# Performance work log

Hardware: AMD Instinct MI355X
Metric: run time of the kernel (lower is better)

## Reference

```python
import jax, jax.numpy as jnp
import numpy as np

N = 2048       # num_nodes
B = 32         # batch
UNITS = 64     # rnn_units
OUT_DIM = 1
K = 2          # max_diffusion_step


def _rw(a):
    # random-walk matrix D^-1 A
    d = a.sum(axis=1, keepdims=True)
    return a / jnp.maximum(d, 1e-8)


def _supports(adj):
    # dual_random_walk: forward and backward random-walk transitions (transposed, as in DCRNN)
    return [_rw(adj).T, _rw(adj.T).T]


def _gconv(supports, x_bnf, w, b):
    # x_bnf: (B, N, F). Faithful to DCRNN: x0 columns are F-major then B,
    # and x0/x1 are rebound across supports exactly like the original loop.
    B_, N_, F_ = x_bnf.shape
    x0 = x_bnf.transpose(1, 2, 0).reshape(N_, F_ * B_)
    xs = [x0]
    for S in supports:
        x1 = S @ x0
        xs.append(x1)
        for _ in range(2, K + 1):
            x2 = 2.0 * (S @ x1) - x0
            xs.append(x2)
            x1, x0 = x2, x1
    M = len(xs)  # num_supports*K + 1 = 5
    x = jnp.stack(xs).reshape(M, N_, F_, B_).transpose(3, 1, 2, 0).reshape(B_ * N_, F_ * M)
    return x @ w + b


def _cell(supports, inp_flat, hx_flat, wg, bg, wc, bc):
    B_ = inp_flat.shape[0]
    inp = inp_flat.reshape(B_, N, -1)
    hx = hx_flat.reshape(B_, N, UNITS)
    cat = jnp.concatenate([inp, hx], axis=-1)
    val = jax.nn.sigmoid(_gconv(supports, cat, wg, bg)).reshape(B_, N, 2 * UNITS)
    r, u = val[..., :UNITS], val[..., UNITS:]
    c = jnp.tanh(_gconv(supports, jnp.concatenate([inp, r * hx], axis=-1), wc, bc).reshape(B_, N, UNITS))
    h = u * hx + (1.0 - u) * c
    return h.reshape(B_, N * UNITS)


def setup_inputs() -> dict:
    key = jax.random.key(0)
    ks = jax.random.split(key, 10)
    s = 0.02
    return {
        "inputs": jax.random.normal(ks[0], (B, N * OUT_DIM), jnp.float32),
        "hidden_state": jax.random.normal(ks[1], (2, B, N * UNITS), jnp.float32),
        "adj_mx": jax.random.uniform(ks[2], (N, N), jnp.float32),
        "w_gate_0": jax.random.normal(ks[3], ((1 + UNITS) * 5, 2 * UNITS), jnp.float32) * s,
        "b_gate_0": jnp.ones((2 * UNITS,), jnp.float32),
        "w_cand_0": jax.random.normal(ks[4], ((1 + UNITS) * 5, UNITS), jnp.float32) * s,
        "b_cand_0": jnp.zeros((UNITS,), jnp.float32),
        "w_gate_1": jax.random.normal(ks[5], ((UNITS + UNITS) * 5, 2 * UNITS), jnp.float32) * s,
        "b_gate_1": jnp.ones((2 * UNITS,), jnp.float32),
        "w_cand_1": jax.random.normal(ks[6], ((UNITS + UNITS) * 5, UNITS), jnp.float32) * s,
        "b_cand_1": jnp.zeros((UNITS,), jnp.float32),
        "w_proj": jax.random.normal(ks[7], (UNITS, OUT_DIM), jnp.float32) * s,
        "b_proj": jnp.zeros((OUT_DIM,), jnp.float32),
    }


def reference(inputs, hidden_state, adj_mx, w_gate_0, b_gate_0, w_cand_0, b_cand_0,
              w_gate_1, b_gate_1, w_cand_1, b_cand_1, w_proj, b_proj):
    supports = _supports(adj_mx)
    h0 = _cell(supports, inputs, hidden_state[0], w_gate_0, b_gate_0, w_cand_0, b_cand_0)
    h1 = _cell(supports, h0, hidden_state[1], w_gate_1, b_gate_1, w_cand_1, b_cand_1)
    out = (h1.reshape(-1, UNITS) @ w_proj + b_proj).reshape(-1, N * OUT_DIM)
    return out, jnp.stack([h0, h1])
```

## Files before the change

### kernel.cpp

```cpp
#include <hip/hip_runtime.h>

typedef unsigned short u16;
typedef unsigned char u8;
typedef unsigned int u32;
typedef float f32x4 __attribute__((ext_vector_type(4)));
typedef __bf16 bf16x8 __attribute__((ext_vector_type(8)));
typedef int i32x8 __attribute__((ext_vector_type(8)));

#define SCL_A 0x77777777
#define SCL_B 0x7F7F7F7F

__device__ __forceinline__ u16 f2bf(float f){
  u32 u = __builtin_bit_cast(u32, f);
  u32 r = (u + 0x7fffu + ((u >> 16) & 1u)) >> 16;
  return (u16)r;
}
__device__ __forceinline__ float bf2f(u16 h){
  return __builtin_bit_cast(float, ((u32)h) << 16);
}
__device__ __forceinline__ u8 f2e4(float x){
  return (u8)(__builtin_amdgcn_cvt_pk_fp8_f32(x, x, 0, false) & 0xff);
}
__device__ __forceinline__ u32 pack4_e4(float a, float b, float c, float d){
  int w = __builtin_amdgcn_cvt_pk_fp8_f32(a, b, 0, false);
  w = __builtin_amdgcn_cvt_pk_fp8_f32(c, d, w, true);
  return (u32)w;
}
__device__ __forceinline__ void gl_lds16(const void* g, void* l){
  __builtin_amdgcn_global_load_lds((__attribute__((address_space(1))) void*)g,
                                   (__attribute__((address_space(3))) void*)l,
                                   16, 0, 0);
}
__device__ __forceinline__ float sigf(float x){ return 1.f/(1.f + __expf(-x)); }

__device__ __forceinline__ void xcd_swizzle(int& x, int& y, int& z){
  int gx = gridDim.x, gy = gridDim.y;
  int nwg = gx * gy * gridDim.z;
  int lid = blockIdx.x + gx*(blockIdx.y + gy*blockIdx.z);
  int cpx = nwg >> 3;
  int swz = (lid & 7)*cpx + (lid >> 3);
  x = swz % gx;
  int rest = swz / gx;
  y = rest % gy;
  z = rest / gy;
}

__global__ __launch_bounds__(256) void k_rowsum(const float* __restrict__ adj, float* __restrict__ inv_rs,
                                                float* __restrict__ cs){
  int j = blockIdx.x; int tid = threadIdx.x;
  float s = 0.f;
  for (int i = tid; i < 2048; i += 256) s += adj[(long)j*2048 + i];
  for (int off = 32; off; off >>= 1) s += __shfl_down(s, off, 64);
  __shared__ float red[4];
  if ((tid & 63) == 0) red[tid >> 6] = s;
  __syncthreads();
  if (tid == 0){
    float t = red[0] + red[1] + red[2] + red[3];
    inv_rs[j] = 1.f / fmaxf(t, 1e-8f);
    cs[j] = 0.f;
  }
}

__global__ __launch_bounds__(256) void k_colsum2(const float* __restrict__ adj, float* __restrict__ cs){
  int j0 = blockIdx.x * 64, i0 = blockIdx.y * 128;
  int jj = threadIdx.x & 63, w = threadIdx.x >> 6;
  float s = 0.f;
  for (int i = w; i < 128; i += 4) s += adj[(long)(i0+i)*2048 + j0 + jj];
  __shared__ float red[256];
  red[threadIdx.x] = s;
  __syncthreads();
  if (w == 0){
    float t = red[jj] + red[64+jj] + red[128+jj] + red[192+jj];
    atomicAdd(&cs[j0+jj], t);
  }
}

__global__ __launch_bounds__(256) void k_build_S(const float* __restrict__ adj,
                                                 const float* __restrict__ inv_rs,
                                                 const float* __restrict__ cs,
                                                 u16* __restrict__ S0, u8* __restrict__ S0q,
                                                 u16* __restrict__ S0T, u16* __restrict__ S1){
  __shared__ float t[64*66];
  __shared__ float rsl[64];
  __shared__ float icl[64];
  int i0 = blockIdx.x * 64, j0 = blockIdx.y * 64;
  int tid = threadIdx.x;
  if (tid < 64) rsl[tid] = inv_rs[j0 + tid];
  else if (tid >= 64 && tid < 128) icl[tid-64] = 1.f / fmaxf(cs[i0 + tid-64], 1e-8f);
  __syncthreads();
  for (int e = tid; e < 4096; e += 256){
    int jj = e >> 6, ii = e & 63;
    float a = adj[(long)(j0+jj)*2048 + i0 + ii];
    t[jj*66 + ii] = a;
    long o = (long)(j0+jj)*2048 + i0 + ii;
    S0T[o] = f2bf(a * rsl[jj]);
    S1[o]  = f2bf(a * icl[ii]);
  }
  __syncthreads();
  for (int e = tid; e < 4096; e += 256){
    int ii = e >> 6, jj = e & 63;
    u16 vb = f2bf(t[jj*66 + ii] * rsl[jj]);
    long o = (long)(i0+ii)*2048 + j0 + jj;
    S0[o] = vb;
    S0q[o] = f2e4(bf2f(vb)*256.f);
  }
}

__global__ __launch_bounds__(256) void k_packW4(const float* __restrict__ wg0, const float* __restrict__ wc0,
                                                const float* __restrict__ wg1, const float* __restrict__ wc1,
                                                u16* __restrict__ WTg0, u16* __restrict__ WTc0,
                                                u16* __restrict__ WTg1, u16* __restrict__ WTc1){
  int z = blockIdx.y;
  const float* w = (z==0) ? wg0 : (z==1) ? wc0 : (z==2) ? wg1 : wc1;
  u16* WT       = (z==0) ? WTg0 : (z==1) ? WTc0 : (z==2) ? WTg1 : WTc1;
  int OUTr = (z==0 || z==2) ? 128 : 64;
  int F  = (z < 2) ? 65 : 128;
  int Fp = (z < 2) ? 72 : 128;
  int Kd = (z < 2) ? 384 : 640;
  int idx = blockIdx.x*256 + threadIdx.x;
  if (idx >= 128*Kd) return;
  int o = idx / Kd, k = idx - o*Kd;
  int m = k / Fp, f = k - m*Fp;
  float v = 0.f;
  if (o < OUTr && m < 5 && f < F) v = w[(long)(f*5 + m)*OUTr + o];
  WT[idx] = f2bf(v);
}

__global__ __launch_bounds__(256) void k_hx_build(const float* __restrict__ hx, const float* __restrict__ inp,
                                                  u8* __restrict__ X0T, u16* __restrict__ D,
                                                  int Fp, int rowoff, long ldD, int coloff, int l0extras){
  __shared__ float t[64*66];
  int b = blockIdx.x, n0 = blockIdx.y * 64;
  int tid = threadIdx.x;
  const float* hb = hx + (long)b*2048*64;
  long bn0 = (long)b*2048 + n0;
  for (int e = tid; e < 4096; e += 256){
    int u = e & 63, ni = e >> 6;
    t[ni*66 + u] = hb[(long)(n0+ni)*64 + u];
  }
  __syncthreads();
  for (int e = tid; e < 4096; e += 256){
    int u = e >> 6, ni = e & 63;
    X0T[((long)b*Fp + rowoff + u)*2048 + n0 + ni] = f2e4(t[ni*66 + u]);
  }
  for (int e = tid; e < 4096; e += 256){
    int ni = e >> 6, u = e & 63;
    D[(bn0 + ni)*ldD + coloff + u] = f2bf(t[ni*66 + u]);
  }
  if (l0extras){
    if (tid < 64){
      float v = inp[(long)b*2048 + n0 + tid];
      X0T[((long)b*Fp)*2048 + n0 + tid] = f2e4(v);
      D[(bn0 + tid)*ldD] = f2bf(v);
    }
    for (int e = tid; e < 7*64; e += 256){
      int f = 65 + (e >> 6), ni = e & 63;
      X0T[((long)b*Fp + f)*2048 + n0 + ni] = 0;
    }
    for (int e = tid; e < 64*31; e += 256){
      int ni = e / 31, wc = e - ni*31;
      int col = (wc < 7) ? (65 + wc) : (353 + wc);
      D[(bn0 + ni)*ldD + col] = 0;
    }
  }
}

__device__ __forceinline__ void gemm_core(const u16* __restrict__ A, const u16* __restrict__ Bt,
                                          int K, long tM, long tC,
                                          u16* lA, u16* lB, f32x4 (&acc)[4][4]){
  int tid = threadIdx.x;
  int wv = tid >> 6, lane = tid & 63;
  int q = lane >> 4, r16 = lane & 15;

  const u16* ga[4]; const u16* gb[4];
  u16* la[4]; u16* lb[4];
  #pragma unroll
  for (int it = 0; it < 4; it++){
    int L = it*256 + tid;
    int r = L >> 3, g = (L & 7) ^ (r & 7);
    ga[it] = A  + (tM + r)*(long)K + g*8;
    gb[it] = Bt + (tC + r)*(long)K + g*8;
    la[it] = lA + (it*256 + wv*64)*8;
    lb[it] = lB + (it*256 + wv*64)*8;
  }

  #pragma unroll
  for (int i = 0; i < 4; i++)
    #pragma unroll
    for (int j = 0; j < 4; j++){ acc[i][j][0]=0.f; acc[i][j][1]=0.f; acc[i][j][2]=0.f; acc[i][j][3]=0.f; }

  int wm = wv & 1, wn = wv >> 1;
  int aoff[4][2], boff[4][2];
  #pragma unroll
  for (int s = 0; s < 4; s++){
    int m = wm*64 + s*16 + r16;
    int n = wn*64 + s*16 + r16;
    #pragma unroll
    for (int h = 0; h < 2; h++){
      aoff[s][h] = (m*8 + ((h*4 + q) ^ (m & 7))) * 8;
      boff[s][h] = (n*8 + ((h*4 + q) ^ (n & 7))) * 8;
    }
  }

  for (int k0 = 0; k0 < K; k0 += 64){
    __syncthreads();
    #pragma unroll
    for (int it = 0; it < 4; it++){
      gl_lds16(ga[it] + k0, la[it]);
      gl_lds16(gb[it] + k0, lb[it]);
    }
    asm volatile("s_waitcnt vmcnt(0)" ::: "memory");
    __syncthreads();
    #pragma unroll
    for (int h = 0; h < 2; h++){
      bf16x8 af[4], bfr[4];
      #pragma unroll
      for (int s = 0; s < 4; s++){
        af[s]  = *(const bf16x8*)&lA[aoff[s][h]];
        bfr[s] = *(const bf16x8*)&lB[boff[s][h]];
      }
      #pragma unroll
      for (int i = 0; i < 4; i++)
        #pragma unroll
        for (int j = 0; j < 4; j++)
          acc[i][j] = __builtin_amdgcn_mfma_f32_16x16x32_bf16(af[i], bfr[j], acc[i][j], 0, 0, 0);
    }
  }
}

__device__ __forceinline__ void gemm_core8(const u8* __restrict__ A, const u8* __restrict__ Bt,
                                           int K, long tM, long tC,
                                           u8* lA, u8* lB, f32x4 (&acc)[4][4]){
  int tid = threadIdx.x;
  int wv = tid >> 6, lane = tid & 63;
  int q = lane >> 4, r16 = lane & 15;

  const u8* ga[4]; const u8* gb[4];
  u8* la[4]; u8* lb[4];
  #pragma unroll
  for (int it = 0; it < 4; it++){
    int L = it*256 + tid;
    int r = L >> 3, x = (L & 7) ^ (r & 7);
    int g = ((x & 3) << 1) | (x >> 2);
    ga[it] = A  + (tM + r)*(long)K + g*16;
    gb[it] = Bt + (tC + r)*(long)K + g*16;
    la[it] = lA + (it*256 + wv*64)*16;
    lb[it] = lB + (it*256 + wv*64)*16;
  }

  #pragma unroll
  for (int i = 0; i < 4; i++)
    #pragma unroll
    for (int j = 0; j < 4; j++){ acc[i][j][0]=0.f; acc[i][j][1]=0.f; acc[i][j][2]=0.f; acc[i][j][3]=0.f; }

  int wm = wv & 1, wn = wv >> 1;
  int aoff[4][2], boff[4][2];
  #pragma unroll
  for (int s = 0; s < 4; s++){
    int m = wm*64 + s*16 + r16;
    int n = wn*64 + s*16 + r16;
    #pragma unroll
    for (int e = 0; e < 2; e++){
      aoff[s][e] = m*128 + ((e*4 + q) ^ (m & 7)) * 16;
      boff[s][e] = n*128 + ((e*4 + q) ^ (n & 7)) * 16;
    }
  }

  for (int k0 = 0; k0 < K; k0 += 128){
    __syncthreads();
    #pragma unroll
    for (int it = 0; it < 4; it++){
      gl_lds16(ga[it] + k0, la[it]);
      gl_lds16(gb[it] + k0, lb[it]);
    }
    asm volatile("s_waitcnt vmcnt(0)" ::: "memory");
    __syncthreads();
    i32x8 af[4], bfr[4];
    #pragma unroll
    for (int s = 0; s < 4; s++){
      uint4 a0 = *(const uint4*)&lA[aoff[s][0]];
      uint4 a1 = *(const uint4*)&lA[aoff[s][1]];
      i32x8 av; av[0]=a0.x; av[1]=a0.y; av[2]=a0.z; av[3]=a0.w; av[4]=a1.x; av[5]=a1.y; av[6]=a1.z; av[7]=a1.w;
      af[s] = av;
      uint4 b0 = *(const uint4*)&lB[boff[s][0]];
      uint4 b1 = *(const uint4*)&lB[boff[s][1]];
      i32x8 bv; bv[0]=b0.x; bv[1]=b0.y; bv[2]=b0.z; bv[3]=b0.w; bv[4]=b1.x; bv[5]=b1.y; bv[6]=b1.z; bv[7]=b1.w;
      bfr[s] = bv;
    }
    #pragma unroll
    for (int i = 0; i < 4; i++)
      #pragma unroll
      for (int j = 0; j < 4; j++)
        acc[i][j] = __builtin_amdgcn_mfma_scale_f32_16x16x128_f8f6f4(
                      af[i], bfr[j], acc[i][j], 0, 0, 0, SCL_A, 0, SCL_B);
  }
}

__global__ __launch_bounds__(256) void gemm_pre(const u16* __restrict__ S0T, const u16* __restrict__ S1,
                                                const u16* __restrict__ S0,
                                                u8* __restrict__ Rq, u16* __restrict__ RT, u8* __restrict__ Vq){
  __shared__ u16 lA[8192];
  __shared__ u16 lB[8192];
  f32x4 acc[4][4];
  int bx, by, bz;
  xcd_swizzle(bx, by, bz);
  const u16* Bt = (bz == 0) ? S1 : S0;
  long tM = (long)bx * 128, tC = (long)by * 128;
  gemm_core(S0T, Bt, 2048, tM, tC, lA, lB, acc);

  int tid = threadIdx.x, wv = tid >> 6, lane = tid & 63;
  int q = lane >> 4, r16 = lane & 15, wm = wv & 1, wn = wv >> 1;
  #pragma unroll
  for (int i = 0; i < 4; i++){
    long gi = tM + wm*64 + i*16 + q*4;
    #pragma unroll
    for (int j = 0; j < 4; j++){
      long gc = tC + wn*64 + j*16 + r16;
      f32x4 v = acc[i][j];
      if (bz == 0){
        *(u32*)(Rq + gc*2048 + gi) = pack4_e4(v[0]*256.f, v[1]*256.f, v[2]*256.f, v[3]*256.f);
        RT[(gi+0)*2048 + gc] = f2bf(v[0]);
        RT[(gi+1)*2048 + gc] = f2bf(v[1]);
        RT[(gi+2)*2048 + gc] = f2bf(v[2]);
        RT[(gi+3)*2048 + gc] = f2bf(v[3]);
      } else {
        float x0 = 2.f*v[0] - ((gi+0) == gc ? 1.f : 0.f);
        float x1 = 2.f*v[1] - ((gi+1) == gc ? 1.f : 0.f);
        float x2 = 2.f*v[2] - ((gi+2) == gc ? 1.f : 0.f);
        float x3 = 2.f*v[3] - ((gi+3) == gc ? 1.f : 0.f);
        *(u32*)(Vq + gc*2048 + gi) = pack4_e4(x0*256.f, x1*256.f, x2*256.f, x3*256.f);
      }
    }
  }
}

__global__ __launch_bounds__(256) void gemm_w(const u16* __restrict__ RT, const u16* __restrict__ S1,
                                              const u16* __restrict__ S0, u8* __restrict__ Wq){
  __shared__ u16 lA[8192];
  __shared__ u16 lB[8192];
  f32x4 acc[4][4];
  int bx, by, bz;
  xcd_swizzle(bx, by, bz);
  long tM = (long)bx * 128, tC = (long)by * 128;
  gemm_core(RT, S1, 2048, tM, tC, lA, lB, acc);

  int tid = threadIdx.x, wv = tid >> 6, lane = tid & 63;
  int q = lane >> 4, r16 = lane & 15, wm = wv & 1, wn = wv >> 1;
  #pragma unroll
  for (int i = 0; i < 4; i++){
    long gi = tM + wm*64 + i*16 + q*4;
    #pragma unroll
    for (int j = 0; j < 4; j++){
      long gc = tC + wn*64 + j*16 + r16;
      f32x4 v = acc[i][j];
      ushort4 x0 = *(const ushort4*)(S0 + gc*2048 + gi);
      *(u32*)(Wq + gc*2048 + gi) = pack4_e4((2.f*v[0] - bf2f(x0.x))*256.f,
                                            (2.f*v[1] - bf2f(x0.y))*256.f,
                                            (2.f*v[2] - bf2f(x0.z))*256.f,
                                            (2.f*v[3] - bf2f(x0.w))*256.f);
    }
  }
}

template<int FP>
__global__ __launch_bounds__(256) void gemm_diff8(const u8* __restrict__ M0, const u8* __restrict__ M1,
                                                  const u8* __restrict__ M2, const u8* __restrict__ M3,
                                                  const u8* __restrict__ X, u16* __restrict__ D, long ldD){
  __shared__ u8 lA[16384];
  __shared__ u8 lB[16384];
  f32x4 acc[4][4];
  int bx, by, z;
  xcd_swizzle(bx, by, z);
  const u8* A = (z == 0) ? M0 : (z == 1) ? M1 : (z == 2) ? M2 : M3;
  long tM = (long)bx * 128, tC = (long)by * 128;
  gemm_core8(A, X, 2048, tM, tC, lA, lB, acc);

  int tid = threadIdx.x, wv = tid >> 6, lane = tid & 63;
  int q = lane >> 4, r16 = lane & 15, wm = wv & 1, wn = wv >> 1;
  int zb = (z + 1) * FP;
  #pragma unroll
  for (int i = 0; i < 4; i++){
    long gi = tM + wm*64 + i*16 + q*4;
    #pragma unroll
    for (int j = 0; j < 4; j++){
      int gc = (int)(tC + wn*64 + j*16 + r16);
      int b = gc / FP, f = gc - b*FP;
      long rb = (long)b*2048 + gi;
      f32x4 v = acc[i][j];
      D[(rb+0)*ldD + zb + f] = f2bf(v[0]);
      D[(rb+1)*ldD + zb + f] = f2bf(v[1]);
      D[(rb+2)*ldD + zb + f] = f2bf(v[2]);
      D[(rb+3)*ldD + zb + f] = f2bf(v[3]);
    }
  }
}

__global__ __launch_bounds__(256) void gemm_diff8_c(const u8* __restrict__ M0, const u8* __restrict__ M1,
                                                    const u8* __restrict__ M2, const u8* __restrict__ M3,
                                                    const u8* __restrict__ Xr, u16* __restrict__ D,
                                                    long ldD, int Fp, int fin){
  __shared__ u8 lA[16384];
  __shared__ u8 lB[16384];
  f32x4 acc[4][4];
  int bx, by, z;
  xcd_swizzle(bx, by, z);
  const u8* A = (z == 0) ? M0 : (z == 1) ? M1 : (z == 2) ? M2 : M3;
  long tM = (long)bx * 128, tC = (long)by * 128;
  gemm_core8(A, Xr, 2048, tM, tC, lA, lB, acc);

  int tid = threadIdx.x, wv = tid >> 6, lane = tid & 63;
  int q = lane >> 4, r16 = lane & 15, wm = wv & 1, wn = wv >> 1;
  int zb = (z + 1) * Fp + fin;
  #pragma unroll
  for (int i = 0; i < 4; i++){
    long gi = tM + wm*64 + i*16 + q*4;
    #pragma unroll
    for (int j = 0; j < 4; j++){
      int gc = (int)(tC + wn*64 + j*16 + r16);
      int b = gc >> 6, u = gc & 63;
      long rb = (long)b*2048 + gi;
      f32x4 v = acc[i][j];
      D[(rb+0)*ldD + zb + u] = f2bf(v[0]);
      D[(rb+1)*ldD + zb + u] = f2bf(v[1]);
      D[(rb+2)*ldD + zb + u] = f2bf(v[2]);
      D[(rb+3)*ldD + zb + u] = f2bf(v[3]);
    }
  }
}

__global__ __launch_bounds__(256) void gemm_dense(const u16* __restrict__ A, const u16* __restrict__ Bt,
                                                  u16* __restrict__ Out, int K, long ldOut){
  __shared__ u16 lA[8192];
  __shared__ u16 lB[8192];
  f32x4 acc[4][4];
  long tM = (long)blockIdx.x * 128, tC = (long)blockIdx.y * 128;
  gemm_core(A, Bt, K, tM, tC, lA, lB, acc);

  int tid = threadIdx.x, wv = tid >> 6, lane = tid & 63;
  int q = lane >> 4, r16 = lane & 15, wm = wv & 1, wn = wv >> 1;
  #pragma unroll
  for (int i = 0; i < 4; i++){
    long gi = tM + wm*64 + i*16 + q*4;
    #pragma unroll
    for (int j = 0; j < 4; j++){
      long gc = tC + wn*64 + j*16 + r16;
      f32x4 v = acc[i][j];
      ushort4 o;
      o.x = f2bf(v[0]); o.y = f2bf(v[1]); o.z = f2bf(v[2]); o.w = f2bf(v[3]);
      *(ushort4*)(Out + gc*ldOut + gi) = o;
    }
  }
}

__global__ __launch_bounds__(256) void k_gate_ep(const u16* __restrict__ GT, const float* __restrict__ bg,
                                                 const float* __restrict__ hid, u8* __restrict__ Xr8,
                                                 u16* __restrict__ D, long ldD, int coloff){
  __shared__ float t[64*66];
  __shared__ u16 tb[64*66];
  int b = blockIdx.x, n0 = blockIdx.y * 64;
  int tid = threadIdx.x;
  long bn0 = (long)b*2048 + n0;
  for (int e = tid; e < 4096; e += 256){
    int u = e & 63, ni = e >> 6;
    t[ni*66 + u] = hid[(bn0 + ni)*64 + u];
  }
  __syncthreads();
  for (int e = tid; e < 4096; e += 256){
    int u = e >> 6, ni = e & 63;
    float r = sigf(bf2f(GT[(long)u*65536 + bn0 + ni]) + bg[u]);
    float pv = r * t[ni*66 + u];
    Xr8[((long)b*64 + u)*2048 + n0 + ni] = f2e4(pv);
    tb[ni*66 + u] = f2bf(pv);
  }
  __syncthreads();
  for (int e = tid; e < 4096; e += 256){
    int ni = e >> 6, u = e & 63;
    D[(bn0 + ni)*ldD + coloff + u] = tb[ni*66 + u];
  }
}

__global__ __launch_bounds__(256) void k_cand_ep(const u16* __restrict__ CT, const u16* __restrict__ GT,
                                                 const float* __restrict__ bc, const float* __restrict__ bg,
                                                 const float* __restrict__ hx, float* __restrict__ hout,
                                                 u8* __restrict__ X0T_next, u16* __restrict__ Dnext,
                                                 const float* __restrict__ wproj, const float* __restrict__ bproj,
                                                 float* __restrict__ out){
  __shared__ u16 tc[64*66];
  __shared__ u16 tu[64*66];
  __shared__ u16 th[64*66];
  int b = blockIdx.x, n0 = blockIdx.y * 64;
  int tid = threadIdx.x;
  long bn0 = (long)b*2048 + n0;
  for (int e = tid; e < 4096; e += 256){
    int u = e >> 6, ni = e & 63;
    float cv = tanhf(bf2f(CT[(long)u*65536 + bn0 + ni]) + bc[u]);
    float uv = sigf(bf2f(GT[(long)(64+u)*65536 + bn0 + ni]) + bg[64+u]);
    tc[ni*66 + u] = f2bf(cv);
    tu[ni*66 + u] = f2bf(uv);
  }
  __syncthreads();
  int lane = tid & 63, wv = tid >> 6;
  for (int it = 0; it < 16; ++it){
    int ni = it*4 + wv, u = lane;
    float hxv = hx[(bn0 + ni)*64 + u];
    float uv = bf2f(tu[ni*66 + u]), cv = bf2f(tc[ni*66 + u]);
    float h = uv*hxv + (1.f - uv)*cv;
    hout[(bn0 + ni)*64 + u] = h;
    if (Dnext) Dnext[(bn0 + ni)*640 + u] = f2bf(h);
    th[ni*66 + u] = f2bf(h);
    if (wproj){
      float v = h * wproj[u];
      for (int off = 32; off; off >>= 1) v += __shfl_down(v, off, 64);
      if (lane == 0) out[(long)b*2048 + n0 + ni] = v + bproj[0];
    }
  }
  __syncthreads();
  if (X0T_next){
    for (int e = tid; e < 4096; e += 256){
      int u = e >> 6, ni = e & 63;
      X0T_next[((long)b*128 + u)*2048 + n0 + ni] = f2e4(bf2f(th[ni*66 + u]));
    }
  }
}

extern "C" void kernel_launch(void* const* d_in, const int* in_sizes, int n_in,
                              void* d_out, int out_size, void* d_ws, size_t ws_size,
                              hipStream_t stream){
  (void)in_sizes; (void)n_in; (void)out_size; (void)ws_size;
  const float* inputs = (const float*)d_in[0];
  const float* hidden = (const float*)d_in[1];
  const float* adj    = (const float*)d_in[2];
  const float* wg0 = (const float*)d_in[3];
  const float* bg0 = (const float*)d_in[4];
  const float* wc0 = (const float*)d_in[5];
  const float* bc0 = (const float*)d_in[6];
  const float* wg1 = (const float*)d_in[7];
  const float* bg1 = (const float*)d_in[8];
  const float* wc1 = (const float*)d_in[9];
  const float* bc1 = (const float*)d_in[10];
  const float* wp  = (const float*)d_in[11];
  const float* bp  = (const float*)d_in[12];
  float* out = (float*)d_out;

  char* p = (char*)d_ws;
  auto alloc = [&](size_t bytes)->char*{ char* r = p; p += (bytes + 255) & ~(size_t)255; return r; };
  float* inv_rs = (float*)alloc(2048*4);
  float* cs     = (float*)alloc(2048*4);
  const size_t SB  = (size_t)2048*2048*2;
  const size_t SB8 = (size_t)2048*2048;
  u16* S0  = (u16*)alloc(SB);
  u16* S0T = (u16*)alloc(SB);
  u16* S1  = (u16*)alloc(SB);
  u16* RT  = (u16*)alloc(SB);
  u8*  S0q = (u8*)alloc(SB8);
  u8*  Rq  = (u8*)alloc(SB8);
  u8*  Vq  = (u8*)alloc(SB8);
  u8*  Wq  = (u8*)alloc(SB8);
  u8*  X0a8 = (u8*)alloc((size_t)2304*2048);
  u8*  X0b8 = (u8*)alloc((size_t)4096*2048);
  u8*  Xr8  = (u8*)alloc(SB8);
  u16* D   = (u16*)alloc((size_t)65536*640*2);
  u16* GT = (u16*)alloc((size_t)128*65536*2);
  u16* CT = (u16*)alloc((size_t)128*65536*2);
  u16* WTg0 = (u16*)alloc((size_t)128*384*2);
  u16* WTc0 = (u16*)alloc((size_t)128*384*2);
  u16* WTg1 = (u16*)alloc((size_t)128*640*2);
  u16* WTc1 = (u16*)alloc((size_t)128*640*2);

  const float* hid0 = hidden;
  const float* hid1 = hidden + (size_t)4194304;
  float* h0out = out + 65536;
  float* h1out = out + 65536 + 4194304;

  k_rowsum<<<2048, 256, 0, stream>>>(adj, inv_rs, cs);
  k_colsum2<<<dim3(32,16), 256, 0, stream>>>(adj, cs);
  k_build_S<<<dim3(32,32), 256, 0, stream>>>(adj, inv_rs, cs, S0, S0q, S0T, S1);
  k_packW4<<<dim3(320,4), 256, 0, stream>>>(wg0, wc0, wg1, wc1, WTg0, WTc0, WTg1, WTc1);
  k_hx_build<<<dim3(32,32), 256, 0, stream>>>(hid0, inputs, X0a8, D, 72, 1, 384, 1, 1);

  gemm_pre<<<dim3(16,16,2), 256, 0, stream>>>(S0T, S1, S0, Rq, RT, Vq);
  gemm_w  <<<dim3(16,16),   256, 0, stream>>>(RT, S1, S0, Wq);

  dim3 gD0(16, 18, 4), gD1(16, 32, 4), gDc(16, 16, 4), gDen(512, 1), gE(32, 32);

  gemm_diff8<72><<<gD0, 256, 0, stream>>>(S0q, Vq, Rq, Wq, X0a8, D, 384);
  gemm_dense<<<gDen, 256, 0, stream>>>(D, WTg0, GT, 384, 65536);
  k_gate_ep<<<gE, 256, 0, stream>>>(GT, bg0, hid0, Xr8, D, 384, 1);

  gemm_diff8_c<<<gDc, 256, 0, stream>>>(S0q, Vq, Rq, Wq, Xr8, D, 384, 72, 1);
  gemm_dense<<<gDen, 256, 0, stream>>>(D, WTc0, CT, 384, 65536);
  k_cand_ep<<<gE, 256, 0, stream>>>(CT, GT, bc0, bg0, hid0, h0out, X0b8, D, nullptr, nullptr, nullptr);

  k_hx_build<<<dim3(32,32), 256, 0, stream>>>(hid1, nullptr, X0b8, D, 128, 64, 640, 64, 0);

  gemm_diff8<128><<<gD1, 256, 0, stream>>>(S0q, Vq, Rq, Wq, X0b8, D, 640);
  gemm_dense<<<gDen, 256, 0, stream>>>(D, WTg1, GT, 640, 65536);
  k_gate_ep<<<gE, 256, 0, stream>>>(GT, bg1, hid1, Xr8, D, 640, 64);

  gemm_diff8_c<<<gDc, 256, 0, stream>>>(S0q, Vq, Rq, Wq, Xr8, D, 640, 128, 64);
  gemm_dense<<<gDen, 256, 0, stream>>>(D, WTc1, CT, 640, 65536);
  k_cand_ep<<<gE, 256, 0, stream>>>(CT, GT, bc1, bg1, hid1, h1out, nullptr, nullptr, wp, bp, out);
}
```

Measured before the change: 575.8 us.

## Replace precomputed W=2*S1*R-S0 matrix with sequential diffusion step on activations

Drops the 2048^3 bf16 gemm_w that built the W operator (and the RT transposed write in gemm_pre). The diffusion step is now computed on activations instead: the z==2 result (R·X) is quantised to fp8 Z2q, and a new fp8 GEMM with S1q produces 2*S1*(R X) - x1, using the already stored x1 in D. This adds four extra dependent GEMM launches of per-cell size, plus fp8 requantisation of an intermediate with a different scale, which may cost accuracy.

Result: slower. 635.3 us (+10.3%).

```diff
diff --git a/kernel.cpp b/kernel.cpp
--- a/kernel.cpp
+++ b/kernel.cpp
@@ -7,8 +7,9 @@
 typedef __bf16 bf16x8 __attribute__((ext_vector_type(8)));
 typedef int i32x8 __attribute__((ext_vector_type(8)));
 
-#define SCL_A 0x77777777
-#define SCL_B 0x7F7F7F7F
+#define SCL_A 0x77777777u
+#define SCL_B1 0x7F7F7F7Fu
+#define SCL_B32 0x7A7A7A7Au
 
 __device__ __forceinline__ u16 f2bf(float f){
   u32 u = __builtin_bit_cast(u32, f);
@@ -79,7 +80,8 @@
                                                  const float* __restrict__ inv_rs,
                                                  const float* __restrict__ cs,
                                                  u16* __restrict__ S0, u8* __restrict__ S0q,
-                                                 u16* __restrict__ S0T, u16* __restrict__ S1){
+                                                 u16* __restrict__ S0T, u16* __restrict__ S1,
+                                                 u8* __restrict__ S1q){
   __shared__ float t[64*66];
   __shared__ float rsl[64];
   __shared__ float icl[64];
@@ -94,7 +96,9 @@
     t[jj*66 + ii] = a;
     long o = (long)(j0+jj)*2048 + i0 + ii;
     S0T[o] = f2bf(a * rsl[jj]);
-    S1[o]  = f2bf(a * icl[ii]);
+    float s1v = a * icl[ii];
+    S1[o]  = f2bf(s1v);
+    S1q[o] = f2e4(s1v * 256.f);
   }
   __syncthreads();
   for (int e = tid; e < 4096; e += 256){
@@ -228,6 +232,7 @@
   }
 }
 
+template<u32 SCLB>
 __device__ __forceinline__ void gemm_core8(const u8* __restrict__ A, const u8* __restrict__ Bt,
                                            int K, long tM, long tC,
                                            u8* lA, u8* lB, f32x4 (&acc)[4][4]){
@@ -292,13 +297,13 @@
       #pragma unroll
       for (int j = 0; j < 4; j++)
         acc[i][j] = __builtin_amdgcn_mfma_scale_f32_16x16x128_f8f6f4(
-                      af[i], bfr[j], acc[i][j], 0, 0, 0, SCL_A, 0, SCL_B);
+                      af[i], bfr[j], acc[i][j], 0, 0, 0, SCL_A, 0, SCLB);
   }
 }
 
 __global__ __launch_bounds__(256) void gemm_pre(const u16* __restrict__ S0T, const u16* __restrict__ S1,
                                                 const u16* __restrict__ S0,
-                                                u8* __restrict__ Rq, u16* __restrict__ RT, u8* __restrict__ Vq){
+                                                u8* __restrict__ Rq, u8* __restrict__ Vq){
   __shared__ u16 lA[8192];
   __shared__ u16 lB[8192];
   f32x4 acc[4][4];
@@ -319,10 +324,6 @@
       f32x4 v = acc[i][j];
       if (bz == 0){
         *(u32*)(Rq + gc*2048 + gi) = pack4_e4(v[0]*256.f, v[1]*256.f, v[2]*256.f, v[3]*256.f);
-        RT[(gi+0)*2048 + gc] = f2bf(v[0]);
-        RT[(gi+1)*2048 + gc] = f2bf(v[1]);
-        RT[(gi+2)*2048 + gc] = f2bf(v[2]);
-        RT[(gi+3)*2048 + gc] = f2bf(v[3]);
       } else {
         float x0 = 2.f*v[0] - ((gi+0) == gc ? 1.f : 0.f);
         float x1 = 2.f*v[1] - ((gi+1) == gc ? 1.f : 0.f);
@@ -334,46 +335,19 @@
   }
 }
 
-__global__ __launch_bounds__(256) void gemm_w(const u16* __restrict__ RT, const u16* __restrict__ S1,
-                                              const u16* __restrict__ S0, u8* __restrict__ Wq){
-  __shared__ u16 lA[8192];
-  __shared__ u16 lB[8192];
-  f32x4 acc[4][4];
-  int bx, by, bz;
-  xcd_swizzle(bx, by, bz);
-  long tM = (long)bx * 128, tC = (long)by * 128;
-  gemm_core(RT, S1, 2048, tM, tC, lA, lB, acc);
-
-  int tid = threadIdx.x, wv = tid >> 6, lane = tid & 63;
-  int q = lane >> 4, r16 = lane & 15, wm = wv & 1, wn = wv >> 1;
-  #pragma unroll
-  for (int i = 0; i < 4; i++){
-    long gi = tM + wm*64 + i*16 + q*4;
-    #pragma unroll
-    for (int j = 0; j < 4; j++){
-      long gc = tC + wn*64 + j*16 + r16;
-      f32x4 v = acc[i][j];
-      ushort4 x0 = *(const ushort4*)(S0 + gc*2048 + gi);
-      *(u32*)(Wq + gc*2048 + gi) = pack4_e4((2.f*v[0] - bf2f(x0.x))*256.f,
-                                            (2.f*v[1] - bf2f(x0.y))*256.f,
-                                            (2.f*v[2] - bf2f(x0.z))*256.f,
-                                            (2.f*v[3] - bf2f(x0.w))*256.f);
-    }
-  }
-}
-
 template<int FP>
 __global__ __launch_bounds__(256) void gemm_diff8(const u8* __restrict__ M0, const u8* __restrict__ M1,
-                                                  const u8* __restrict__ M2, const u8* __restrict__ M3,
-                                                  const u8* __restrict__ X, u16* __restrict__ D, long ldD){
+                                                  const u8* __restrict__ M2,
+                                                  const u8* __restrict__ X, u16* __restrict__ D, long ldD,
+                                                  u8* __restrict__ Z2q){
   __shared__ u8 lA[16384];
   __shared__ u8 lB[16384];
   f32x4 acc[4][4];
   int bx, by, z;
   xcd_swizzle(bx, by, z);
-  const u8* A = (z == 0) ? M0 : (z == 1) ? M1 : (z == 2) ? M2 : M3;
+  const u8* A = (z == 0) ? M0 : (z == 1) ? M1 : M2;
   long tM = (long)bx * 128, tC = (long)by * 128;
-  gemm_core8(A, X, 2048, tM, tC, lA, lB, acc);
+  gemm_core8<SCL_B1>(A, X, 2048, tM, tC, lA, lB, acc);
 
   int tid = threadIdx.x, wv = tid >> 6, lane = tid & 63;
   int q = lane >> 4, r16 = lane & 15, wm = wv & 1, wn = wv >> 1;
@@ -391,22 +365,24 @@
       D[(rb+1)*ldD + zb + f] = f2bf(v[1]);
       D[(rb+2)*ldD + zb + f] = f2bf(v[2]);
       D[(rb+3)*ldD + zb + f] = f2bf(v[3]);
+      if (z == 2)
+        *(u32*)(Z2q + (long)gc*2048 + gi) = pack4_e4(v[0]*32.f, v[1]*32.f, v[2]*32.f, v[3]*32.f);
     }
   }
 }
 
 __global__ __launch_bounds__(256) void gemm_diff8_c(const u8* __restrict__ M0, const u8* __restrict__ M1,
-                                                    const u8* __restrict__ M2, const u8* __restrict__ M3,
+                                                    const u8* __restrict__ M2,
                                                     const u8* __restrict__ Xr, u16* __restrict__ D,
-                                                    long ldD, int Fp, int fin){
+                                                    long ldD, int Fp, int fin, u8* __restrict__ Z2q){
   __shared__ u8 lA[16384];
   __shared__ u8 lB[16384];
   f32x4 acc[4][4];
   int bx, by, z;
   xcd_swizzle(bx, by, z);
-  const u8* A = (z == 0) ? M0 : (z == 1) ? M1 : (z == 2) ? M2 : M3;
+  const u8* A = (z == 0) ? M0 : (z == 1) ? M1 : M2;
   long tM = (long)bx * 128, tC = (long)by * 128;
-  gemm_core8(A, Xr, 2048, tM, tC, lA, lB, acc);
+  gemm_core8<SCL_B1>(A, Xr, 2048, tM, tC, lA, lB, acc);
 
   int tid = threadIdx.x, wv = tid >> 6, lane = tid & 63;
   int q = lane >> 4, r16 = lane & 15, wm = wv & 1, wn = wv >> 1;
@@ -424,6 +400,69 @@
       D[(rb+1)*ldD + zb + u] = f2bf(v[1]);
       D[(rb+2)*ldD + zb + u] = f2bf(v[2]);
       D[(rb+3)*ldD + zb + u] = f2bf(v[3]);
+      if (z == 2)
+        *(u32*)(Z2q + (long)gc*2048 + gi) = pack4_e4(v[0]*32.f, v[1]*32.f, v[2]*32.f, v[3]*32.f);
+    }
+  }
+}
+
+template<int FP>
+__global__ __launch_bounds__(256) void gemm_diff8w(const u8* __restrict__ S1q, const u8* __restrict__ Z2q,
+                                                   u16* __restrict__ D, long ldD){
+  __shared__ u8 lA[16384];
+  __shared__ u8 lB[16384];
+  f32x4 acc[4][4];
+  int bx, by, bz;
+  xcd_swizzle(bx, by, bz);
+  long tM = (long)bx * 128, tC = (long)by * 128;
+  gemm_core8<SCL_B32>(S1q, Z2q, 2048, tM, tC, lA, lB, acc);
+
+  int tid = threadIdx.x, wv = tid >> 6, lane = tid & 63;
+  int q = lane >> 4, r16 = lane & 15, wm = wv & 1, wn = wv >> 1;
+  int zb = 4 * FP;
+  #pragma unroll
+  for (int i = 0; i < 4; i++){
+    long gi = tM + wm*64 + i*16 + q*4;
+    #pragma unroll
+    for (int j = 0; j < 4; j++){
+      int gc = (int)(tC + wn*64 + j*16 + r16);
+      int b = gc / FP, f = gc - b*FP;
+      long rb = (long)b*2048 + gi;
+      f32x4 v = acc[i][j];
+      D[(rb+0)*ldD + zb + f] = f2bf(2.f*v[0] - bf2f(D[(rb+0)*ldD + FP + f]));
+      D[(rb+1)*ldD + zb + f] = f2bf(2.f*v[1] - bf2f(D[(rb+1)*ldD + FP + f]));
+      D[(rb+2)*ldD + zb + f] = f2bf(2.f*v[2] - bf2f(D[(rb+2)*ldD + FP + f]));
+      D[(rb+3)*ldD + zb + f] = f2bf(2.f*v[3] - bf2f(D[(rb+3)*ldD + FP + f]));
+    }
+  }
+}
+
+__global__ __launch_bounds__(256) void gemm_diff8w_c(const u8* __restrict__ S1q, const u8* __restrict__ Z2q,
+                                                     u16* __restrict__ D, long ldD, int Fp, int fin){
+  __shared__ u8 lA[16384];
+  __shared__ u8 lB[16384];
+  f32x4 acc[4][4];
+  int bx, by, bz;
+  xcd_swizzle(bx, by, bz);
+  long tM = (long)bx * 128, tC = (long)by * 128;
+  gemm_core8<SCL_B32>(S1q, Z2q, 2048, tM, tC, lA, lB, acc);
+
+  int tid = threadIdx.x, wv = tid >> 6, lane = tid & 63;
+  int q = lane >> 4, r16 = lane & 15, wm = wv & 1, wn = wv >> 1;
+  int zb = 4*Fp + fin, z0b = Fp + fin;
+  #pragma unroll
+  for (int i = 0; i < 4; i++){
+    long gi = tM + wm*64 + i*16 + q*4;
+    #pragma unroll
+    for (int j = 0; j < 4; j++){
+      int gc = (int)(tC + wn*64 + j*16 + r16);
+      int b = gc >> 6, u = gc & 63;
+      long rb = (long)b*2048 + gi;
+      f32x4 v = acc[i][j];
+      D[(rb+0)*ldD + zb + u] = f2bf(2.f*v[0] - bf2f(D[(rb+0)*ldD + z0b + u]));
+      D[(rb+1)*ldD + zb + u] = f2bf(2.f*v[1] - bf2f(D[(rb+1)*ldD + z0b + u]));
+      D[(rb+2)*ldD + zb + u] = f2bf(2.f*v[2] - bf2f(D[(rb+2)*ldD + z0b + u]));
+      D[(rb+3)*ldD + zb + u] = f2bf(2.f*v[3] - bf2f(D[(rb+3)*ldD + z0b + u]));
     }
   }
 }
@@ -551,11 +590,11 @@
   u16* S0  = (u16*)alloc(SB);
   u16* S0T = (u16*)alloc(SB);
   u16* S1  = (u16*)alloc(SB);
-  u16* RT  = (u16*)alloc(SB);
   u8*  S0q = (u8*)alloc(SB8);
+  u8*  S1q = (u8*)alloc(SB8);
   u8*  Rq  = (u8*)alloc(SB8);
   u8*  Vq  = (u8*)alloc(SB8);
-  u8*  Wq  = (u8*)alloc(SB8);
+  u8*  Z2q = (u8*)alloc((size_t)4096*2048);
   u8*  X0a8 = (u8*)alloc((size_t)2304*2048);
   u8*  X0b8 = (u8*)alloc((size_t)4096*2048);
   u8*  Xr8  = (u8*)alloc(SB8);
@@ -574,30 +613,35 @@
 
   k_rowsum<<<2048, 256, 0, stream>>>(adj, inv_rs, cs);
   k_colsum2<<<dim3(32,16), 256, 0, stream>>>(adj, cs);
-  k_build_S<<<dim3(32,32), 256, 0, stream>>>(adj, inv_rs, cs, S0, S0q, S0T, S1);
+  k_build_S<<<dim3(32,32), 256, 0, stream>>>(adj, inv_rs, cs, S0, S0q, S0T, S1, S1q);
   k_packW4<<<dim3(320,4), 256, 0, stream>>>(wg0, wc0, wg1, wc1, WTg0, WTc0, WTg1, WTc1);
   k_hx_build<<<dim3(32,32), 256, 0, stream>>>(hid0, inputs, X0a8, D, 72, 1, 384, 1, 1);
 
-  gemm_pre<<<dim3(16,16,2), 256, 0, stream>>>(S0T, S1, S0, Rq, RT, Vq);
-  gemm_w  <<<dim3(16,16),   256, 0, stream>>>(RT, S1, S0, Wq);
-
-  dim3 gD0(16, 18, 4), gD1(16, 32, 4), gDc(16, 16, 4), gDen(512, 1), gE(32, 32);
-
-  gemm_diff8<72><<<gD0, 256, 0, stream>>>(S0q, Vq, Rq, Wq, X0a8, D, 384);
+  gemm_pre<<<dim3(16,16,2), 256, 0, stream>>>(S0T, S1, S0, Rq, Vq);
+
+  dim3 gD0(16, 18, 3), gD1(16, 32, 3), gDc(16, 16, 3);
+  dim3 gW0(16, 18), gW1(16, 32), gWc(16, 16);
+  dim3 gDen(512, 1), gE(32, 32);
+
+  gemm_diff8<72><<<gD0, 256, 0, stream>>>(S0q, Vq, Rq, X0a8, D, 384, Z2q);
+  gemm_diff8w<72><<<gW0, 256, 0, stream>>>(S1q, Z2q, D, 384);
   gemm_dense<<<gDen, 256, 0, stream>>>(D, WTg0, GT, 384, 65536);
   k_gate_ep<<<gE, 256, 0, stream>>>(GT, bg0, hid0, Xr8, D, 384, 1);
 
-  gemm_diff8_c<<<gDc, 256, 0, stream>>>(S0q, Vq, Rq, Wq, Xr8, D, 384, 72, 1);
+  gemm_diff8_c<<<gDc, 256, 0, stream>>>(S0q, Vq, Rq, Xr8, D, 384, 72, 1, Z2q);
+  gemm_diff8w_c<<<gWc, 256, 0, stream>>>(S1q, Z2q, D, 384, 72, 1);
   gemm_dense<<<gDen, 256, 0, stream>>>(D, WTc0, CT, 384, 65536);
   k_cand_ep<<<gE, 256, 0, stream>>>(CT, GT, bc0, bg0, hid0, h0out, X0b8, D, nullptr, nullptr, nullptr);
 
   k_hx_build<<<dim3(32,32), 256, 0, stream>>>(hid1, nullptr, X0b8, D, 128, 64, 640, 64, 0);
 
-  gemm_diff8<128><<<gD1, 256, 0, stream>>>(S0q, Vq, Rq, Wq, X0b8, D, 640);
+  gemm_diff8<128><<<gD1, 256, 0, stream>>>(S0q, Vq, Rq, X0b8, D, 640, Z2q);
+  gemm_diff8w<128><<<gW1, 256, 0, stream>>>(S1q, Z2q, D, 640);
   gemm_dense<<<gDen, 256, 0, stream>>>(D, WTg1, GT, 640, 65536);
   k_gate_ep<<<gE, 256, 0, stream>>>(GT, bg1, hid1, Xr8, D, 640, 64);
 
-  gemm_diff8_c<<<gDc, 256, 0, stream>>>(S0q, Vq, Rq, Wq, Xr8, D, 640, 128, 64);
+  gemm_diff8_c<<<gDc, 256, 0, stream>>>(S0q, Vq, Rq, Xr8, D, 640, 128, 64, Z2q);
+  gemm_diff8w_c<<<gWc, 256, 0, stream>>>(S1q, Z2q, D, 640, 128, 64);
   gemm_dense<<<gDen, 256, 0, stream>>>(D, WTc1, CT, 640, 65536);
   k_cand_ep<<<gE, 256, 0, stream>>>(CT, GT, bc1, bg1, hid1, h1out, nullptr, nullptr, wp, bp, out);
 }
```
